# Kernel tuning notes

Measured on AMD Instinct MI355X. Metric: run time of the kernel, lower is better.

Reference implementation:

```python
import jax, jax.numpy as jnp
import numpy as np

K = 2  # top-k experts selected per token (config['k'])
SPARSITY_EPS = 1e-05


def setup_inputs() -> dict:
    key = jax.random.key(0)
    k1, k2, k3 = jax.random.split(key, 3)
    N, D, E = 8192, 768, 16  # tokens, hidden dim, num experts
    f = jax.random.normal(k1, (N, D, E), dtype=jnp.float32)   # stacked expert outputs
    x = jax.random.normal(k2, (N, D), dtype=jnp.float32)      # routing inputs
    W = jax.random.normal(k3, (E, D), dtype=jnp.float32) * 0.02  # gate Linear weight
    b = jnp.zeros((E,), dtype=jnp.float32)                    # gate Linear bias
    return {"f": f, "x": x, "W": W, "b": b}


def reference(f, x, W, b):
    # gate logits: [N, E]
    gate_logits = x @ W.T + b
    N, E = gate_logits.shape

    # top-k selection + softmax over selected logits.
    # scatter(-inf) then softmax over the full expert axis is mathematically
    # identical to softmax over the k selected values scattered back to zeros.
    vals, idx = jax.lax.top_k(gate_logits, K)          # [N, K], [N, K]
    w = jax.nn.softmax(vals, axis=-1)                  # [N, K]
    rows = jnp.arange(N)[:, None]                      # [N, 1]
    g = jnp.zeros((N, E), gate_logits.dtype).at[rows, idx].set(w)[..., None]  # [N, E, 1]

    # batched expert combine: [N, D, E] @ [N, E, 1] -> [N, D]
    y = jnp.matmul(f, g)[..., 0]

    # metrics (the ones returned by the torch forward)
    s_concat = jnp.where(g < SPARSITY_EPS, 1.0, 0.0).astype(g.dtype)  # [N, E, 1]
    soft_averages = jnp.mean(g, axis=0)                               # [E, 1]
    hard_averages = jnp.mean(1.0 - s_concat, axis=0)                  # [E, 1]

    return (y, soft_averages, hard_averages, s_concat, 0)
```

## Files before the change

### kernel.cpp

```cpp
#include <hip/hip_runtime.h>
#include <math.h>

#define N_TOK 8192
#define DDIM  768
#define NEXP  16
#define WPAD  17

typedef float f32x4 __attribute__((ext_vector_type(4)));

#define SOFT_OFF (N_TOK*DDIM)
#define HARD_OFF (SOFT_OFF + NEXP)
#define S_OFF    (HARD_OFF + NEXP)
#define SCAL_OFF (S_OFF + N_TOK*NEXP)

extern "C" __global__ void init_ws_kernel(float* __restrict__ ws) {
  if (threadIdx.x < 32) ws[threadIdx.x] = 0.0f;
}

__device__ __forceinline__ void fma4(f32x4& a, float s, f32x4 w) {
  a.x = fmaf(s, w.x, a.x);
  a.y = fmaf(s, w.y, a.y);
  a.z = fmaf(s, w.z, a.z);
  a.w = fmaf(s, w.w, a.w);
}

__device__ __forceinline__ float xred(float v) {
  v += __shfl_xor(v, 4);
  v += __shfl_xor(v, 8);
  v += __shfl_xor(v, 16);
  v += __shfl_xor(v, 32);
  return v;
}

__device__ __forceinline__ void finish_token(
    int n, f32x4 av, int lane, float* __restrict__ out,
    f32x4* __restrict__ table, float* s_soft, float* s_hard) {
  float v[16];
  #pragma unroll
  for (int q = 0; q < 4; ++q) {
    v[q*4+0] = __shfl(av.x, q);
    v[q*4+1] = __shfl(av.y, q);
    v[q*4+2] = __shfl(av.z, q);
    v[q*4+3] = __shfl(av.w, q);
  }
  float v0 = -INFINITY, v1 = -INFINITY;
  int e0 = 0, e1 = 0;
  #pragma unroll
  for (int j = 0; j < 16; ++j) {
    float val = v[j];
    if (val > v0) { v1 = v0; e1 = e0; v0 = val; e0 = j; }
    else if (val > v1) { v1 = val; e1 = j; }
  }
  float t1  = expf(v1 - v0);
  float inv = 1.0f / (1.0f + t1);
  float w0  = inv;
  float w1  = t1 * inv;
  if (lane == 0) {
    f32x4 rec;
    rec.x = __int_as_float(e0); rec.y = __int_as_float(e1);
    rec.z = w0; rec.w = w1;
    table[n] = rec;
  }
  if (lane < NEXP) {
    float g  = (lane == e0) ? w0 : ((lane == e1) ? w1 : 0.0f);
    bool sel = (g >= 1e-5f);
    out[S_OFF + (size_t)n*NEXP + lane] = sel ? 0.0f : 1.0f;
    atomicAdd(&s_soft[lane], g);
    if (sel) atomicAdd(&s_hard[lane], 1.0f);
  }
}

extern "C" __global__ __launch_bounds__(256) void gate_kernel(
    const float* __restrict__ x, const float* __restrict__ W,
    const float* __restrict__ bias, float* __restrict__ out,
    float* __restrict__ ws) {
  __shared__ float Wl[DDIM*WPAD];
  __shared__ float s_soft[NEXP];
  __shared__ float s_hard[NEXP];
  f32x4* table = (f32x4*)(ws + 32);
  int tid = threadIdx.x;
  if (tid < NEXP) { s_soft[tid] = 0.0f; s_hard[tid] = 0.0f; }
  for (int idx = tid; idx < DDIM*NEXP; idx += 256) {
    int e = idx / DDIM;
    int d = idx - e*DDIM;
    Wl[d*WPAD + e] = W[idx];
  }
  __syncthreads();

  int wave = tid >> 6;
  int lane = tid & 63;
  int e4 = lane & 3;
  int c  = lane >> 2;
  f32x4 bq = ((const f32x4*)bias)[e4];

  #pragma unroll
  for (int p = 0; p < 2; ++p) {
    int pairi = (blockIdx.x*4 + wave) + p*2048;
    int n0 = pairi*2, n1 = n0 + 1;
    const float* x0p = x + (size_t)n0*DDIM + c*48;
    const float* x1p = x + (size_t)n1*DDIM + c*48;
    const float* wbase = &Wl[(c*48)*WPAD + 4*e4];
    f32x4 a0 = {0.f,0.f,0.f,0.f};
    f32x4 a1 = {0.f,0.f,0.f,0.f};
    #pragma unroll
    for (int m = 0; m < 12; ++m) {
      f32x4 xv0 = *(const f32x4*)(x0p + 4*m);
      f32x4 xv1 = *(const f32x4*)(x1p + 4*m);
      const float* wb = wbase + m*4*WPAD;
      f32x4 wq0 = *(const f32x4*)(wb);
      f32x4 wq1 = *(const f32x4*)(wb + WPAD);
      f32x4 wq2 = *(const f32x4*)(wb + 2*WPAD);
      f32x4 wq3 = *(const f32x4*)(wb + 3*WPAD);
      fma4(a0, xv0.x, wq0); fma4(a0, xv0.y, wq1);
      fma4(a0, xv0.z, wq2); fma4(a0, xv0.w, wq3);
      fma4(a1, xv1.x, wq0); fma4(a1, xv1.y, wq1);
      fma4(a1, xv1.z, wq2); fma4(a1, xv1.w, wq3);
    }
    a0.x = xred(a0.x); a0.y = xred(a0.y); a0.z = xred(a0.z); a0.w = xred(a0.w);
    a1.x = xred(a1.x); a1.y = xred(a1.y); a1.z = xred(a1.z); a1.w = xred(a1.w);
    a0.x += bq.x; a0.y += bq.y; a0.z += bq.z; a0.w += bq.w;
    a1.x += bq.x; a1.y += bq.y; a1.z += bq.z; a1.w += bq.w;
    finish_token(n0, a0, lane, out, table, s_soft, s_hard);
    finish_token(n1, a1, lane, out, table, s_soft, s_hard);
  }
  __syncthreads();
  if (tid < NEXP) {
    atomicAdd(&ws[tid], s_soft[tid]);
    atomicAdd(&ws[NEXP + tid], s_hard[tid]);
  }
}

extern "C" __global__ __launch_bounds__(256) void combine_kernel(
    const float* __restrict__ f, const float* __restrict__ ws,
    float* __restrict__ out) {
  __shared__ float part[DDIM*4];
  const int n   = blockIdx.x;
  const int tid = threadIdx.x;

  if (n == 0) {
    if (tid < 32) out[SOFT_OFF + tid] = ws[tid] * (1.0f/N_TOK);
    if (tid == 0) out[SCAL_OFF] = 0.0f;
  }

  f32x4 rec = ((const f32x4*)(ws + 32))[n];
  int e0 = __float_as_int(rec.x);
  int e1 = __float_as_int(rec.y);
  float w0 = rec.z, w1 = rec.w;
  const int jg = (tid & 3) * 4;
  float gx = (jg+0 == e0) ? w0 : ((jg+0 == e1) ? w1 : 0.0f);
  float gy = (jg+1 == e0) ? w0 : ((jg+1 == e1) ? w1 : 0.0f);
  float gz = (jg+2 == e0) ? w0 : ((jg+2 == e1) ? w1 : 0.0f);
  float gw = (jg+3 == e0) ? w0 : ((jg+3 == e1) ? w1 : 0.0f);

  const f32x4* fp = (const f32x4*)(f + (size_t)n * (DDIM*NEXP));
  #pragma unroll
  for (int k = 0; k < 12; ++k) {
    int q = tid + 256*k;
    f32x4 v = fp[q];
    part[q] = v.x*gx + v.y*gy + v.z*gz + v.w*gw;
  }
  __syncthreads();

  float* yr = out + (size_t)n * DDIM;
  #pragma unroll
  for (int i = 0; i < 3; ++i) {
    int d = tid + 256*i;
    f32x4 pv = ((const f32x4*)part)[d];
    yr[d] = (pv.x + pv.y) + (pv.z + pv.w);
  }
}

extern "C" void kernel_launch(void* const* d_in, const int* in_sizes, int n_in,
                              void* d_out, int out_size, void* d_ws, size_t ws_size,
                              hipStream_t stream) {
  const float* f = (const float*)d_in[0];
  const float* x = (const float*)d_in[1];
  const float* W = (const float*)d_in[2];
  const float* b = (const float*)d_in[3];
  float* out = (float*)d_out;
  float* ws  = (float*)d_ws;

  hipLaunchKernelGGL(init_ws_kernel, dim3(1), dim3(64), 0, stream, ws);
  hipLaunchKernelGGL(gate_kernel, dim3(512), dim3(256), 0, stream,
                     x, W, b, out, ws);
  hipLaunchKernelGGL(combine_kernel, dim3(N_TOK), dim3(256), 0, stream,
                     f, ws, out);
}
```

Measured before the change: 118.5 us.

## Drop atomics and init kernel; compute metrics in combine block, shuffle-reduce combine

Removes the init kernel and all shared/global atomics for the soft/hard averages. Block 0 of the combine kernel now recomputes these averages by scanning the routing table. The combine kernel processes four tokens per block and replaces the shared-memory partial buffer with lane shuffles. The goal is less launch and atomic overhead and fewer blocks, at the cost of a serial 512-iteration metric scan in one block and narrower scattered stores to y.

```diff
diff --git a/kernel.cpp b/kernel.cpp
--- a/kernel.cpp
+++ b/kernel.cpp
@@ -13,9 +13,6 @@
 #define S_OFF    (HARD_OFF + NEXP)
 #define SCAL_OFF (S_OFF + N_TOK*NEXP)
 
-extern "C" __global__ void init_ws_kernel(float* __restrict__ ws) {
-  if (threadIdx.x < 32) ws[threadIdx.x] = 0.0f;
-}
 
 __device__ __forceinline__ void fma4(f32x4& a, float s, f32x4 w) {
   a.x = fmaf(s, w.x, a.x);
@@ -34,7 +31,7 @@
 
 __device__ __forceinline__ void finish_token(
     int n, f32x4 av, int lane, float* __restrict__ out,
-    f32x4* __restrict__ table, float* s_soft, float* s_hard) {
+    f32x4* __restrict__ table) {
   float v[16];
   #pragma unroll
   for (int q = 0; q < 4; ++q) {
@@ -63,10 +60,7 @@
   }
   if (lane < NEXP) {
     float g  = (lane == e0) ? w0 : ((lane == e1) ? w1 : 0.0f);
-    bool sel = (g >= 1e-5f);
-    out[S_OFF + (size_t)n*NEXP + lane] = sel ? 0.0f : 1.0f;
-    atomicAdd(&s_soft[lane], g);
-    if (sel) atomicAdd(&s_hard[lane], 1.0f);
+    out[S_OFF + (size_t)n*NEXP + lane] = (g >= 1e-5f) ? 0.0f : 1.0f;
   }
 }
 
@@ -75,11 +69,8 @@
     const float* __restrict__ bias, float* __restrict__ out,
     float* __restrict__ ws) {
   __shared__ float Wl[DDIM*WPAD];
-  __shared__ float s_soft[NEXP];
-  __shared__ float s_hard[NEXP];
-  f32x4* table = (f32x4*)(ws + 32);
+  f32x4* table = (f32x4*)ws;
   int tid = threadIdx.x;
-  if (tid < NEXP) { s_soft[tid] = 0.0f; s_hard[tid] = 0.0f; }
   for (int idx = tid; idx < DDIM*NEXP; idx += 256) {
     int e = idx / DDIM;
     int d = idx - e*DDIM;
@@ -120,53 +111,64 @@
     a1.x = xred(a1.x); a1.y = xred(a1.y); a1.z = xred(a1.z); a1.w = xred(a1.w);
     a0.x += bq.x; a0.y += bq.y; a0.z += bq.z; a0.w += bq.w;
     a1.x += bq.x; a1.y += bq.y; a1.z += bq.z; a1.w += bq.w;
-    finish_token(n0, a0, lane, out, table, s_soft, s_hard);
-    finish_token(n1, a1, lane, out, table, s_soft, s_hard);
-  }
-  __syncthreads();
-  if (tid < NEXP) {
-    atomicAdd(&ws[tid], s_soft[tid]);
-    atomicAdd(&ws[NEXP + tid], s_hard[tid]);
+    finish_token(n0, a0, lane, out, table);
+    finish_token(n1, a1, lane, out, table);
   }
 }
 
 extern "C" __global__ __launch_bounds__(256) void combine_kernel(
     const float* __restrict__ f, const float* __restrict__ ws,
     float* __restrict__ out) {
-  __shared__ float part[DDIM*4];
-  const int n   = blockIdx.x;
   const int tid = threadIdx.x;
+  const f32x4* table = (const f32x4*)ws;
+  __shared__ float red[4][2*NEXP];
 
-  if (n == 0) {
-    if (tid < 32) out[SOFT_OFF + tid] = ws[tid] * (1.0f/N_TOK);
+  if (blockIdx.x == 0) {
+    const int wv = tid >> 6, lane = tid & 63;
+    const int e = lane & 15, h = lane >> 4;
+    float asoft = 0.f, ahard = 0.f;
+    for (int i = 0; i < 512; ++i) {
+      f32x4 rec = table[wv*2048 + 4*i + h];
+      int e0 = __float_as_int(rec.x);
+      int e1 = __float_as_int(rec.y);
+      float g = (e == e0) ? rec.z : ((e == e1) ? rec.w : 0.0f);
+      asoft += g;
+      ahard += (g >= 1e-5f) ? 1.0f : 0.0f;
+    }
+    asoft += __shfl_xor(asoft, 16); asoft += __shfl_xor(asoft, 32);
+    ahard += __shfl_xor(ahard, 16); ahard += __shfl_xor(ahard, 32);
+    if (lane < NEXP) { red[wv][e] = asoft; red[wv][NEXP + e] = ahard; }
+    __syncthreads();
+    if (tid < 2*NEXP) {
+      float s = red[0][tid] + red[1][tid] + red[2][tid] + red[3][tid];
+      out[SOFT_OFF + tid] = s * (1.0f/N_TOK);
+    }
     if (tid == 0) out[SCAL_OFF] = 0.0f;
   }
 
-  f32x4 rec = ((const f32x4*)(ws + 32))[n];
-  int e0 = __float_as_int(rec.x);
-  int e1 = __float_as_int(rec.y);
-  float w0 = rec.z, w1 = rec.w;
   const int jg = (tid & 3) * 4;
-  float gx = (jg+0 == e0) ? w0 : ((jg+0 == e1) ? w1 : 0.0f);
-  float gy = (jg+1 == e0) ? w0 : ((jg+1 == e1) ? w1 : 0.0f);
-  float gz = (jg+2 == e0) ? w0 : ((jg+2 == e1) ? w1 : 0.0f);
-  float gw = (jg+3 == e0) ? w0 : ((jg+3 == e1) ? w1 : 0.0f);
-
-  const f32x4* fp = (const f32x4*)(f + (size_t)n * (DDIM*NEXP));
-  #pragma unroll
-  for (int k = 0; k < 12; ++k) {
-    int q = tid + 256*k;
-    f32x4 v = fp[q];
-    part[q] = v.x*gx + v.y*gy + v.z*gz + v.w*gw;
-  }
-  __syncthreads();
-
-  float* yr = out + (size_t)n * DDIM;
-  #pragma unroll
-  for (int i = 0; i < 3; ++i) {
-    int d = tid + 256*i;
-    f32x4 pv = ((const f32x4*)part)[d];
-    yr[d] = (pv.x + pv.y) + (pv.z + pv.w);
+  #pragma unroll 1
+  for (int t = 0; t < 4; ++t) {
+    const int n = blockIdx.x*4 + t;
+    f32x4 rec = table[n];
+    int e0 = __float_as_int(rec.x);
+    int e1 = __float_as_int(rec.y);
+    float w0 = rec.z, w1 = rec.w;
+    float gx = (jg+0 == e0) ? w0 : ((jg+0 == e1) ? w1 : 0.0f);
+    float gy = (jg+1 == e0) ? w0 : ((jg+1 == e1) ? w1 : 0.0f);
+    float gz = (jg+2 == e0) ? w0 : ((jg+2 == e1) ? w1 : 0.0f);
+    float gw = (jg+3 == e0) ? w0 : ((jg+3 == e1) ? w1 : 0.0f);
+    const f32x4* fp = (const f32x4*)(f + (size_t)n * (DDIM*NEXP));
+    float* yr = out + (size_t)n * DDIM;
+    #pragma unroll
+    for (int k = 0; k < 12; ++k) {
+      int q = tid + 256*k;
+      f32x4 v = fp[q];
+      float p = v.x*gx + v.y*gy + v.z*gz + v.w*gw;
+      p += __shfl_xor(p, 1);
+      p += __shfl_xor(p, 2);
+      if ((tid & 3) == 0) yr[q >> 2] = p;
+    }
   }
 }
 
@@ -180,9 +182,8 @@
   float* out = (float*)d_out;
   float* ws  = (float*)d_ws;
 
-  hipLaunchKernelGGL(init_ws_kernel, dim3(1), dim3(64), 0, stream, ws);
   hipLaunchKernelGGL(gate_kernel, dim3(512), dim3(256), 0, stream,
                      x, W, b, out, ws);
-  hipLaunchKernelGGL(combine_kernel, dim3(N_TOK), dim3(256), 0, stream,
+  hipLaunchKernelGGL(combine_kernel, dim3(2048), dim3(256), 0, stream,
                      f, ws, out);
 }
```

New measurement: 148.7 us. 1.25x slower.
